# Kernel optimization log

Hardware: AMD Instinct MI355X
Metric: run time of the kernel (lower is better)

## Reference

```python
import jax, jax.numpy as jnp
import numpy as np

HIDDEN = 1024
HEADS = 16
HEAD = HIDDEN // HEADS


def setup_inputs() -> dict:
    key = jax.random.key(0)
    ks = jax.random.split(key, 6)
    B, T = 2, 2048
    x = jax.random.normal(ks[0], (B, T, HIDDEN), dtype=jnp.float32)
    mask = jnp.ones((T, T), dtype=jnp.float32)
    s = 1.0 / np.sqrt(HIDDEN)
    Wqkv = jax.random.normal(ks[1], (HIDDEN, 3 * HIDDEN), dtype=jnp.float32) * s
    bqkv = jnp.zeros((3 * HIDDEN,), dtype=jnp.float32)
    Wproj = jax.random.normal(ks[2], (HIDDEN, HIDDEN), dtype=jnp.float32) * s
    bproj = jnp.zeros((HIDDEN,), dtype=jnp.float32)
    return {"x": x, "mask": mask, "Wqkv": Wqkv, "bqkv": bqkv,
            "Wproj": Wproj, "bproj": bproj}


def reference(x, mask, Wqkv, bqkv, Wproj, bproj):
    B, T, C = x.shape
    qkv = x @ Wqkv + bqkv                      # [B,T,3C]
    q, k, v = jnp.split(qkv, 3, axis=-1)
    def heads(t):                              # [B,T,C] -> [B,H,T,D]
        return t.reshape(B, T, HEADS, HEAD).transpose(0, 2, 1, 3)
    q, k, v = heads(q), heads(k), heads(v)
    scores = jnp.einsum('bhqd,bhkd->bhqk', q, k) / np.sqrt(HEAD)
    scores = jnp.where(mask == 0, -jnp.inf, scores)
    attn = jax.nn.softmax(scores, axis=-1)
    out = jnp.einsum('bhqk,bhkd->bhqd', attn, v)
    out = out.transpose(0, 2, 1, 3).reshape(B, T, C)
    return out @ Wproj + bproj
```

## Files before the change

### kernel.cpp

```cpp
#include <hip/hip_runtime.h>
#include <stdint.h>

#define HID 1024
#define NH 16
#define HD 64
#define BATCH 2
#define SEQ 2048
#define MR (BATCH*SEQ)
#define NQKV (3*HID)

typedef __attribute__((ext_vector_type(8))) _Float16 h16x8;
typedef __attribute__((ext_vector_type(2))) __fp16 fp16x2;
typedef __attribute__((ext_vector_type(8))) unsigned short u16x8;
typedef __attribute__((ext_vector_type(4))) float f32x4;

#if __has_builtin(__builtin_amdgcn_exp2f)
#define EXP2(x) __builtin_amdgcn_exp2f(x)
#else
#define EXP2(x) exp2f(x)
#endif

static __device__ __forceinline__ unsigned short f2h(float f) {
  union { _Float16 h; unsigned short u; } v; v.h = (_Float16)f; return v.u;
}
static __device__ __forceinline__ unsigned pk2(float a, float b) {
  union { fp16x2 h; unsigned u; } v;
  v.h = __builtin_amdgcn_cvt_pkrtz(a, b);
  return v.u;
}

typedef const __attribute__((address_space(1))) unsigned int glb_u32;
typedef __attribute__((address_space(3))) unsigned int lds_u32;
static __device__ __forceinline__ void cp16(const void* g, void* l) {
  __builtin_amdgcn_global_load_lds((glb_u32*)g, (lds_u32*)l, 16, 0, 0);
}

#define QSCL (0.125f * 1.44269504f)

__global__ __launch_bounds__(256) void k_prep(const float4* __restrict__ x4,
                                              const float* __restrict__ mask,
                                              const float* __restrict__ Wqkv,
                                              const float* __restrict__ Wproj,
                                              ushort4* __restrict__ xh,
                                              unsigned short* __restrict__ WqT,
                                              unsigned short* __restrict__ WpT,
                                              unsigned long long* __restrict__ mb) {
  __shared__ float tile[32][33];
  int blk = blockIdx.x, tid = threadIdx.x;
  if (blk < 4096) {
    int i = blk * 256 + tid;
    float4 v = x4[i];
    ushort4 h;
    h.x = f2h(v.x); h.y = f2h(v.y); h.z = f2h(v.z); h.w = f2h(v.w);
    xh[i] = h;
  } else if (blk < 8192) {
    const float* src; unsigned short* dst; int C, bx, by;
    if (blk < 7168) { src = Wqkv;  dst = WqT; C = NQKV; int b2 = blk - 4096; bx = b2 % 96; by = b2 / 96; }
    else            { src = Wproj; dst = WpT; C = HID;  int b2 = blk - 7168; bx = b2 & 31; by = b2 >> 5; }
    int tx = tid & 31, ty = tid >> 5;
    int col0 = bx * 32, row0 = by * 32;
    #pragma unroll
    for (int i = 0; i < 32; i += 8)
      tile[ty + i][tx] = src[(size_t)(row0 + ty + i) * C + col0 + tx];
    __syncthreads();
    #pragma unroll
    for (int i = 0; i < 32; i += 8)
      dst[(size_t)(col0 + ty + i) * HID + row0 + tx] = f2h(tile[tx][ty + i]);
  } else {
    int gw = (blk - 8192) * 4 + (tid >> 6);
    int lane = tid & 63;
    float v = mask[(size_t)gw * 64 + lane];
    unsigned long long b = __ballot(v != 0.f);
    if (lane == 0) mb[gw] = b;
  }
}

__global__ __launch_bounds__(256) void k_gemm_qkv(const unsigned short* __restrict__ A,
                                                  const unsigned short* __restrict__ Bt,
                                                  const float* __restrict__ bias,
                                                  unsigned short* __restrict__ Qp,
                                                  unsigned short* __restrict__ Kp,
                                                  unsigned short* __restrict__ Vt) {
  const int K = HID;
  int tid = threadIdx.x;
  int wave = tid >> 6, lane = tid & 63, quad = lane >> 4, l16 = lane & 15;
  int wm = wave >> 1, wn = wave & 1;
  int x7 = l16 & 7;
  int m0 = blockIdx.y * 128, n0 = blockIdx.x * 128;
  __shared__ __align__(16) unsigned short As[128 * 64], Bs[128 * 64];
  f32x4 acc[4][4] = {};
  for (int k0 = 0; k0 < K; k0 += 64) {
    __syncthreads();
    #pragma unroll
    for (int i = 0; i < 4; i++) {
      int c = tid + i * 256;
      int r = c >> 3, sc = ((c ^ r) & 7) << 3;
      cp16(&A[(size_t)(m0 + r) * K + k0 + sc], &As[c << 3]);
      cp16(&Bt[(size_t)(n0 + r) * K + k0 + sc], &Bs[c << 3]);
    }
    __syncthreads();
    #pragma unroll
    for (int kc = 0; kc < 2; kc++) {
      h16x8 af[4], bf[4];
      #pragma unroll
      for (int i = 0; i < 4; i++) {
        af[i] = *(const h16x8*)&As[(wm * 64 + i * 16 + l16) * 64 + (((kc * 4 + quad) ^ x7) << 3)];
        bf[i] = *(const h16x8*)&Bs[(wn * 64 + i * 16 + l16) * 64 + (((kc * 4 + quad) ^ x7) << 3)];
      }
      #pragma unroll
      for (int i = 0; i < 4; i++)
        #pragma unroll
        for (int j = 0; j < 4; j++)
          acc[i][j] = __builtin_amdgcn_mfma_f32_16x16x32_f16(af[i], bf[j], acc[i][j], 0, 0, 0);
    }
  }
  #pragma unroll
  for (int j = 0; j < 4; j++) {
    int n = n0 + wn * 64 + j * 16 + l16;
    float bv = bias[n];
    int which = n >> 10;
    int rem = n & 1023;
    int h = rem >> 6, d = rem & 63;
    if (which == 2) {
      #pragma unroll
      for (int i = 0; i < 4; i++) {
        int m = m0 + wm * 64 + i * 16 + quad * 4;
        int b = m >> 11, t = m & 2047;
        uint2 tt;
        tt.x = pk2(acc[i][j][0] + bv, acc[i][j][1] + bv);
        tt.y = pk2(acc[i][j][2] + bv, acc[i][j][3] + bv);
        *(uint2*)&Vt[(size_t)(b * NH + h) * (SEQ * HD) + (size_t)d * SEQ + t] = tt;
      }
    } else {
      #pragma unroll
      for (int i = 0; i < 4; i++)
        #pragma unroll
        for (int r = 0; r < 4; r++) {
          int m = m0 + wm * 64 + i * 16 + quad * 4 + r;
          int b = m >> 11, t = m & 2047;
          float val = acc[i][j][r] + bv;
          int hb = b * NH + h;
          if (which == 0) Qp[(size_t)hb * (SEQ * HD) + (size_t)t * HD + d] = f2h(val * QSCL);
          else            Kp[(size_t)hb * (SEQ * HD) + (size_t)t * HD + d] = f2h(val);
        }
    }
  }
}

__global__ __launch_bounds__(256) void k_attn(const unsigned short* __restrict__ Qp,
                                              const unsigned short* __restrict__ Kp,
                                              const unsigned short* __restrict__ Vt,
                                              const unsigned long long* __restrict__ mb,
                                              unsigned short* __restrict__ AO) {
  int tid = threadIdx.x, wave = tid >> 6, lane = tid & 63, quad = lane >> 4, l16 = lane & 15;
  int bh = blockIdx.y, qbase = blockIdx.x * 128;
  const unsigned short* Qg = Qp + (size_t)bh * (SEQ * HD);
  const unsigned short* Kg = Kp + (size_t)bh * (SEQ * HD);
  const unsigned short* Vg = Vt + (size_t)bh * (SEQ * HD);
  __shared__ __align__(16) unsigned short smem[20992];
  unsigned short* Qs = smem;
  unsigned short* Ks = smem + 8192;
  unsigned short* Vs = smem + 12288;
  unsigned short* Ps = smem + 16384 + wave * (16 * 72);
  unsigned short* Os = smem;

  #pragma unroll
  for (int i = 0; i < 4; i++) {
    int c = tid + i * 256;
    int row = c >> 3, sc = ((c ^ row) & 7) << 3;
    cp16(&Qg[(size_t)(qbase + row) * HD + sc], &Qs[c << 3]);
  }
  int q0 = qbase + wave * 32 + l16;
  const unsigned long long* mrow0 = mb + (size_t)q0 * 32;
  const unsigned long long* mrow1 = mb + (size_t)(q0 + 16) * 32;
  f32x4 acc_o[2][4] = {};
  f32x4 acc_l[2] = {};
  int x7 = l16 & 7;

  h16x8 vone;
  #pragma unroll
  for (int j = 0; j < 8; j++) vone[j] = (_Float16)1.0f;

  __syncthreads();
  h16x8 bq[2][2];
  #pragma unroll
  for (int s = 0; s < 2; s++)
    #pragma unroll
    for (int kk = 0; kk < 2; kk++)
      bq[s][kk] = *(const h16x8*)&Qs[(wave * 32 + s * 16 + l16) * 64 + (((kk * 4 + quad) ^ x7) << 3)];

  for (int kt = 0; kt < 32; kt++) {
    int kbase = kt * 64;
    __syncthreads();
    #pragma unroll
    for (int i = 0; i < 2; i++) {
      int c = tid + i * 256;
      int row = c >> 3, sc = ((c ^ row) & 7) << 3;
      cp16(&Kg[(size_t)(kbase + row) * HD + sc], &Ks[c << 3]);
      cp16(&Vg[(size_t)row * SEQ + kbase + sc], &Vs[c << 3]);
    }
    unsigned long long w0 = mrow0[kt], w1 = mrow1[kt];
    __syncthreads();
    h16x8 ka[4][2];
    #pragma unroll
    for (int nt = 0; nt < 4; nt++)
      #pragma unroll
      for (int kk = 0; kk < 2; kk++)
        ka[nt][kk] = *(const h16x8*)&Ks[(nt * 16 + l16) * 64 + (((kk * 4 + quad) ^ x7) << 3)];
    f32x4 s0[4] = {}, s1[4] = {};
    #pragma unroll
    for (int nt = 0; nt < 4; nt++)
      #pragma unroll
      for (int kk = 0; kk < 2; kk++) {
        s0[nt] = __builtin_amdgcn_mfma_f32_16x16x32_f16(ka[nt][kk], bq[0][kk], s0[nt], 0, 0, 0);
        s1[nt] = __builtin_amdgcn_mfma_f32_16x16x32_f16(ka[nt][kk], bq[1][kk], s1[nt], 0, 0, 0);
      }
    if (!__all((w0 & w1) == ~0ULL)) {
      #pragma unroll
      for (int nt = 0; nt < 4; nt++)
        #pragma unroll
        for (int r = 0; r < 4; r++) {
          int bit = nt * 16 + quad * 4 + r;
          if (!((w0 >> bit) & 1ULL)) s0[nt][r] = -100.f;
          if (!((w1 >> bit) & 1ULL)) s1[nt][r] = -100.f;
        }
    }
    #pragma unroll
    for (int nt = 0; nt < 4; nt++)
      #pragma unroll
      for (int r = 0; r < 4; r++) {
        s0[nt][r] = EXP2(s0[nt][r]);
        s1[nt][r] = EXP2(s1[nt][r]);
      }
    h16x8 va[4][2];
    #pragma unroll
    for (int nt = 0; nt < 4; nt++)
      #pragma unroll
      for (int kk = 0; kk < 2; kk++)
        va[nt][kk] = *(const h16x8*)&Vs[(nt * 16 + l16) * 64 + (((kk * 4 + quad) ^ x7) << 3)];
    #pragma unroll
    for (int nt = 0; nt < 4; nt++) {
      uint2 t;
      t.x = pk2(s0[nt][0], s0[nt][1]);
      t.y = pk2(s0[nt][2], s0[nt][3]);
      *(uint2*)&Ps[l16 * 72 + nt * 16 + quad * 4] = t;
    }
    {
      h16x8 bp0 = *(const h16x8*)&Ps[l16 * 72 + quad * 8];
      h16x8 bp1 = *(const h16x8*)&Ps[l16 * 72 + 32 + quad * 8];
      acc_l[0] = __builtin_amdgcn_mfma_f32_16x16x32_f16(vone, bp0, acc_l[0], 0, 0, 0);
      acc_l[0] = __builtin_amdgcn_mfma_f32_16x16x32_f16(vone, bp1, acc_l[0], 0, 0, 0);
      #pragma unroll
      for (int nt = 0; nt < 4; nt++) {
        acc_o[0][nt] = __builtin_amdgcn_mfma_f32_16x16x32_f16(va[nt][0], bp0, acc_o[0][nt], 0, 0, 0);
        acc_o[0][nt] = __builtin_amdgcn_mfma_f32_16x16x32_f16(va[nt][1], bp1, acc_o[0][nt], 0, 0, 0);
      }
    }
    #pragma unroll
    for (int nt = 0; nt < 4; nt++) {
      uint2 t;
      t.x = pk2(s1[nt][0], s1[nt][1]);
      t.y = pk2(s1[nt][2], s1[nt][3]);
      *(uint2*)&Ps[l16 * 72 + nt * 16 + quad * 4] = t;
    }
    {
      h16x8 bp0 = *(const h16x8*)&Ps[l16 * 72 + quad * 8];
      h16x8 bp1 = *(const h16x8*)&Ps[l16 * 72 + 32 + quad * 8];
      acc_l[1] = __builtin_amdgcn_mfma_f32_16x16x32_f16(vone, bp0, acc_l[1], 0, 0, 0);
      acc_l[1] = __builtin_amdgcn_mfma_f32_16x16x32_f16(vone, bp1, acc_l[1], 0, 0, 0);
      #pragma unroll
      for (int nt = 0; nt < 4; nt++) {
        acc_o[1][nt] = __builtin_amdgcn_mfma_f32_16x16x32_f16(va[nt][0], bp0, acc_o[1][nt], 0, 0, 0);
        acc_o[1][nt] = __builtin_amdgcn_mfma_f32_16x16x32_f16(va[nt][1], bp1, acc_o[1][nt], 0, 0, 0);
      }
    }
  }
  float rl0 = 1.0f / acc_l[0][0];
  float rl1 = 1.0f / acc_l[1][0];
  __syncthreads();
  #pragma unroll
  for (int nt = 0; nt < 4; nt++) {
    uint2 t;
    t.x = (unsigned)f2h(acc_o[0][nt][0] * rl0) | ((unsigned)f2h(acc_o[0][nt][1] * rl0) << 16);
    t.y = (unsigned)f2h(acc_o[0][nt][2] * rl0) | ((unsigned)f2h(acc_o[0][nt][3] * rl0) << 16);
    *(uint2*)&Os[(wave * 32 + l16) * 72 + nt * 16 + quad * 4] = t;
    uint2 u;
    u.x = (unsigned)f2h(acc_o[1][nt][0] * rl1) | ((unsigned)f2h(acc_o[1][nt][1] * rl1) << 16);
    u.y = (unsigned)f2h(acc_o[1][nt][2] * rl1) | ((unsigned)f2h(acc_o[1][nt][3] * rl1) << 16);
    *(uint2*)&Os[(wave * 32 + 16 + l16) * 72 + nt * 16 + quad * 4] = u;
  }
  __syncthreads();
  int b = bh >> 4, h = bh & 15;
  #pragma unroll
  for (int i = 0; i < 4; i++) {
    int c = tid + i * 256;
    int row = c >> 3, co = (c & 7) << 3;
    u16x8 vv = *(const u16x8*)&Os[row * 72 + co];
    *(u16x8*)&AO[(size_t)(b * SEQ + qbase + row) * HID + h * HD + co] = vv;
  }
}

__global__ __launch_bounds__(256) void k_gemm_proj(const unsigned short* __restrict__ A,
                                                   const unsigned short* __restrict__ Bt,
                                                   const float* __restrict__ bias,
                                                   float* __restrict__ out) {
  const int K = HID;
  int tid = threadIdx.x;
  int wave = tid >> 6, lane = tid & 63, quad = lane >> 4, l16 = lane & 15;
  int wm = wave >> 1, wn = wave & 1;
  int x7 = l16 & 7;
  int m0 = blockIdx.y * 128, n0 = blockIdx.x * 64;
  __shared__ __align__(16) unsigned short As[128 * 64], Bs[64 * 64];
  f32x4 acc[4][2] = {};
  for (int k0 = 0; k0 < K; k0 += 64) {
    __syncthreads();
    #pragma unroll
    for (int i = 0; i < 4; i++) {
      int c = tid + i * 256;
      int r = c >> 3, sc = ((c ^ r) & 7) << 3;
      cp16(&A[(size_t)(m0 + r) * K + k0 + sc], &As[c << 3]);
    }
    #pragma unroll
    for (int i = 0; i < 2; i++) {
      int c = tid + i * 256;
      int r = c >> 3, sc = ((c ^ r) & 7) << 3;
      cp16(&Bt[(size_t)(n0 + r) * K + k0 + sc], &Bs[c << 3]);
    }
    __syncthreads();
    #pragma unroll
    for (int kc = 0; kc < 2; kc++) {
      h16x8 af[4], bf[2];
      #pragma unroll
      for (int i = 0; i < 4; i++)
        af[i] = *(const h16x8*)&As[(wm * 64 + i * 16 + l16) * 64 + (((kc * 4 + quad) ^ x7) << 3)];
      #pragma unroll
      for (int j = 0; j < 2; j++)
        bf[j] = *(const h16x8*)&Bs[(wn * 32 + j * 16 + l16) * 64 + (((kc * 4 + quad) ^ x7) << 3)];
      #pragma unroll
      for (int i = 0; i < 4; i++)
        #pragma unroll
        for (int j = 0; j < 2; j++)
          acc[i][j] = __builtin_amdgcn_mfma_f32_16x16x32_f16(af[i], bf[j], acc[i][j], 0, 0, 0);
    }
  }
  #pragma unroll
  for (int j = 0; j < 2; j++) {
    int n = n0 + wn * 32 + j * 16 + l16;
    float bv = bias[n];
    #pragma unroll
    for (int i = 0; i < 4; i++)
      #pragma unroll
      for (int r = 0; r < 4; r++) {
        int m = m0 + wm * 64 + i * 16 + quad * 4 + r;
        out[(size_t)m * HID + n] = acc[i][j][r] + bv;
      }
  }
}

extern "C" void kernel_launch(void* const* d_in, const int* in_sizes, int n_in,
                              void* d_out, int out_size, void* d_ws, size_t ws_size,
                              hipStream_t stream) {
  const float* x     = (const float*)d_in[0];
  const float* mask  = (const float*)d_in[1];
  const float* Wqkv  = (const float*)d_in[2];
  const float* bqkv  = (const float*)d_in[3];
  const float* Wproj = (const float*)d_in[4];
  const float* bproj = (const float*)d_in[5];
  float* out = (float*)d_out;

  uint8_t* ws = (uint8_t*)d_ws;
  size_t off = 0;
  auto alloc = [&](size_t bytes) -> void* {
    void* p = (void*)(ws + off);
    off += (bytes + 255) & ~(size_t)255;
    return p;
  };
  unsigned short* xh   = (unsigned short*)alloc((size_t)MR * HID * 2);
  unsigned short* WqT  = (unsigned short*)alloc((size_t)NQKV * HID * 2);
  unsigned short* WpT  = (unsigned short*)alloc((size_t)HID * HID * 2);
  unsigned short* Qp   = (unsigned short*)alloc((size_t)BATCH * NH * SEQ * HD * 2);
  unsigned short* Kp   = (unsigned short*)alloc((size_t)BATCH * NH * SEQ * HD * 2);
  unsigned short* Vtp  = (unsigned short*)alloc((size_t)BATCH * NH * SEQ * HD * 2);
  unsigned short* AO   = (unsigned short*)alloc((size_t)MR * HID * 2);
  unsigned long long* mb = (unsigned long long*)alloc((size_t)SEQ * (SEQ / 64) * 8);

  k_prep<<<24576, 256, 0, stream>>>((const float4*)x, mask, Wqkv, Wproj,
                                    (ushort4*)xh, WqT, WpT, mb);
  k_gemm_qkv<<<dim3(NQKV / 128, MR / 128), 256, 0, stream>>>(xh, WqT, bqkv, Qp, Kp, Vtp);
  k_attn<<<dim3(SEQ / 128, BATCH * NH), 256, 0, stream>>>(Qp, Kp, Vtp, mb, AO);
  k_gemm_proj<<<dim3(HID / 64, MR / 128), 256, 0, stream>>>(AO, WpT, bproj, out);
}
```

Baseline: 218.0 us.

## Double-buffer K/V tiles and feed P to MFMA from registers

The attention kernel now prefetches the next K/V tile into a second LDS buffer while the current tile is computed, with one barrier per iteration instead of two. The P matrix no longer round-trips through LDS: the 16x16x16 MFMA variant lets the fp32 scores be packed straight into the B-operand registers, and V is read as 4-wide fragments to match. It also raises wave priority around the MFMA blocks. The cost is more LDS, a larger count of smaller MFMAs, and manual waitcnt/barrier handling, which drops the sync before the output staging that reuses smem.

```diff
diff --git a/kernel.cpp b/kernel.cpp
--- a/kernel.cpp
+++ b/kernel.cpp
@@ -10,6 +10,7 @@
 #define NQKV (3*HID)
 
 typedef __attribute__((ext_vector_type(8))) _Float16 h16x8;
+typedef __attribute__((ext_vector_type(4))) _Float16 h16x4;
 typedef __attribute__((ext_vector_type(2))) __fp16 fp16x2;
 typedef __attribute__((ext_vector_type(8))) unsigned short u16x8;
 typedef __attribute__((ext_vector_type(4))) float f32x4;
@@ -157,11 +158,8 @@
   const unsigned short* Qg = Qp + (size_t)bh * (SEQ * HD);
   const unsigned short* Kg = Kp + (size_t)bh * (SEQ * HD);
   const unsigned short* Vg = Vt + (size_t)bh * (SEQ * HD);
-  __shared__ __align__(16) unsigned short smem[20992];
+  __shared__ __align__(16) unsigned short smem[24576];
   unsigned short* Qs = smem;
-  unsigned short* Ks = smem + 8192;
-  unsigned short* Vs = smem + 12288;
-  unsigned short* Ps = smem + 16384 + wave * (16 * 72);
   unsigned short* Os = smem;
 
   #pragma unroll
@@ -169,6 +167,13 @@
     int c = tid + i * 256;
     int row = c >> 3, sc = ((c ^ row) & 7) << 3;
     cp16(&Qg[(size_t)(qbase + row) * HD + sc], &Qs[c << 3]);
+  }
+  #pragma unroll
+  for (int i = 0; i < 2; i++) {
+    int c = tid + i * 256;
+    int row = c >> 3, sc = ((c ^ row) & 7) << 3;
+    cp16(&Kg[(size_t)row * HD + sc], &smem[8192 + (c << 3)]);
+    cp16(&Vg[(size_t)row * SEQ + sc], &smem[12288 + (c << 3)]);
   }
   int q0 = qbase + wave * 32 + l16;
   const unsigned long long* mrow0 = mb + (size_t)q0 * 32;
@@ -177,9 +182,9 @@
   f32x4 acc_l[2] = {};
   int x7 = l16 & 7;
 
-  h16x8 vone;
-  #pragma unroll
-  for (int j = 0; j < 8; j++) vone[j] = (_Float16)1.0f;
+  h16x4 vone4;
+  #pragma unroll
+  for (int j = 0; j < 4; j++) vone4[j] = (_Float16)1.0f;
 
   __syncthreads();
   h16x8 bq[2][2];
@@ -190,24 +195,27 @@
       bq[s][kk] = *(const h16x8*)&Qs[(wave * 32 + s * 16 + l16) * 64 + (((kk * 4 + quad) ^ x7) << 3)];
 
   for (int kt = 0; kt < 32; kt++) {
-    int kbase = kt * 64;
-    __syncthreads();
-    #pragma unroll
-    for (int i = 0; i < 2; i++) {
-      int c = tid + i * 256;
-      int row = c >> 3, sc = ((c ^ row) & 7) << 3;
-      cp16(&Kg[(size_t)(kbase + row) * HD + sc], &Ks[c << 3]);
-      cp16(&Vg[(size_t)row * SEQ + kbase + sc], &Vs[c << 3]);
+    unsigned short* cb = smem + 8192 + ((kt & 1) << 13);
+    if (kt < 31) {
+      unsigned short* nb = smem + 8192 + (((kt + 1) & 1) << 13);
+      int kb2 = (kt + 1) * 64;
+      #pragma unroll
+      for (int i = 0; i < 2; i++) {
+        int c = tid + i * 256;
+        int row = c >> 3, sc = ((c ^ row) & 7) << 3;
+        cp16(&Kg[(size_t)(kb2 + row) * HD + sc], &nb[c << 3]);
+        cp16(&Vg[(size_t)row * SEQ + kb2 + sc], &nb[4096 + (c << 3)]);
+      }
     }
     unsigned long long w0 = mrow0[kt], w1 = mrow1[kt];
-    __syncthreads();
     h16x8 ka[4][2];
     #pragma unroll
     for (int nt = 0; nt < 4; nt++)
       #pragma unroll
       for (int kk = 0; kk < 2; kk++)
-        ka[nt][kk] = *(const h16x8*)&Ks[(nt * 16 + l16) * 64 + (((kk * 4 + quad) ^ x7) << 3)];
+        ka[nt][kk] = *(const h16x8*)&cb[(nt * 16 + l16) * 64 + (((kk * 4 + quad) ^ x7) << 3)];
     f32x4 s0[4] = {}, s1[4] = {};
+    __builtin_amdgcn_s_setprio(1);
     #pragma unroll
     for (int nt = 0; nt < 4; nt++)
       #pragma unroll
@@ -215,6 +223,15 @@
         s0[nt] = __builtin_amdgcn_mfma_f32_16x16x32_f16(ka[nt][kk], bq[0][kk], s0[nt], 0, 0, 0);
         s1[nt] = __builtin_amdgcn_mfma_f32_16x16x32_f16(ka[nt][kk], bq[1][kk], s1[nt], 0, 0, 0);
       }
+    __builtin_amdgcn_s_setprio(0);
+    h16x4 va16[4][4];
+    #pragma unroll
+    for (int nt = 0; nt < 4; nt++)
+      #pragma unroll
+      for (int seg = 0; seg < 4; seg++)
+        va16[nt][seg] = *(const h16x4*)&cb[4096 + (nt * 16 + l16) * 64 +
+                                           (((seg * 2 + (quad >> 1)) ^ x7) << 3) +
+                                           ((quad & 1) << 2)];
     if (!__all((w0 & w1) == ~0ULL)) {
       #pragma unroll
       for (int nt = 0; nt < 4; nt++)
@@ -232,52 +249,28 @@
         s0[nt][r] = EXP2(s0[nt][r]);
         s1[nt][r] = EXP2(s1[nt][r]);
       }
-    h16x8 va[4][2];
-    #pragma unroll
-    for (int nt = 0; nt < 4; nt++)
-      #pragma unroll
-      for (int kk = 0; kk < 2; kk++)
-        va[nt][kk] = *(const h16x8*)&Vs[(nt * 16 + l16) * 64 + (((kk * 4 + quad) ^ x7) << 3)];
-    #pragma unroll
-    for (int nt = 0; nt < 4; nt++) {
-      uint2 t;
-      t.x = pk2(s0[nt][0], s0[nt][1]);
-      t.y = pk2(s0[nt][2], s0[nt][3]);
-      *(uint2*)&Ps[l16 * 72 + nt * 16 + quad * 4] = t;
-    }
-    {
-      h16x8 bp0 = *(const h16x8*)&Ps[l16 * 72 + quad * 8];
-      h16x8 bp1 = *(const h16x8*)&Ps[l16 * 72 + 32 + quad * 8];
-      acc_l[0] = __builtin_amdgcn_mfma_f32_16x16x32_f16(vone, bp0, acc_l[0], 0, 0, 0);
-      acc_l[0] = __builtin_amdgcn_mfma_f32_16x16x32_f16(vone, bp1, acc_l[0], 0, 0, 0);
-      #pragma unroll
-      for (int nt = 0; nt < 4; nt++) {
-        acc_o[0][nt] = __builtin_amdgcn_mfma_f32_16x16x32_f16(va[nt][0], bp0, acc_o[0][nt], 0, 0, 0);
-        acc_o[0][nt] = __builtin_amdgcn_mfma_f32_16x16x32_f16(va[nt][1], bp1, acc_o[0][nt], 0, 0, 0);
-      }
-    }
-    #pragma unroll
-    for (int nt = 0; nt < 4; nt++) {
-      uint2 t;
-      t.x = pk2(s1[nt][0], s1[nt][1]);
-      t.y = pk2(s1[nt][2], s1[nt][3]);
-      *(uint2*)&Ps[l16 * 72 + nt * 16 + quad * 4] = t;
-    }
-    {
-      h16x8 bp0 = *(const h16x8*)&Ps[l16 * 72 + quad * 8];
-      h16x8 bp1 = *(const h16x8*)&Ps[l16 * 72 + 32 + quad * 8];
-      acc_l[1] = __builtin_amdgcn_mfma_f32_16x16x32_f16(vone, bp0, acc_l[1], 0, 0, 0);
-      acc_l[1] = __builtin_amdgcn_mfma_f32_16x16x32_f16(vone, bp1, acc_l[1], 0, 0, 0);
-      #pragma unroll
-      for (int nt = 0; nt < 4; nt++) {
-        acc_o[1][nt] = __builtin_amdgcn_mfma_f32_16x16x32_f16(va[nt][0], bp0, acc_o[1][nt], 0, 0, 0);
-        acc_o[1][nt] = __builtin_amdgcn_mfma_f32_16x16x32_f16(va[nt][1], bp1, acc_o[1][nt], 0, 0, 0);
-      }
-    }
+    auto pv = [&](const f32x4 (&s)[4], f32x4 (&ao)[4], f32x4 &al) {
+      #pragma unroll
+      for (int seg = 0; seg < 4; seg++) {
+        union { h16x4 h; unsigned u[2]; } pb;
+        pb.u[0] = pk2(s[seg][0], s[seg][1]);
+        pb.u[1] = pk2(s[seg][2], s[seg][3]);
+        al = __builtin_amdgcn_mfma_f32_16x16x16f16(vone4, pb.h, al, 0, 0, 0);
+        #pragma unroll
+        for (int nt = 0; nt < 4; nt++)
+          ao[nt] = __builtin_amdgcn_mfma_f32_16x16x16f16(va16[nt][seg], pb.h, ao[nt], 0, 0, 0);
+      }
+    };
+    __builtin_amdgcn_s_setprio(1);
+    pv(s0, acc_o[0], acc_l[0]);
+    pv(s1, acc_o[1], acc_l[1]);
+    __builtin_amdgcn_s_setprio(0);
+    asm volatile("s_waitcnt vmcnt(0)" ::: "memory");
+    __builtin_amdgcn_s_barrier();
+    __builtin_amdgcn_sched_barrier(0);
   }
   float rl0 = 1.0f / acc_l[0][0];
   float rl1 = 1.0f / acc_l[1][0];
-  __syncthreads();
   #pragma unroll
   for (int nt = 0; nt < 4; nt++) {
     uint2 t;
```

Result: faster. 208.9 us (-4.2%).
